# Kernel optimization log

Hardware: AMD Instinct MI355X
Metric: run time of the kernel (lower is better)

## Reference

```python
import jax, jax.numpy as jnp
import numpy as np

SHARPNESS_SIGMA = 0.75
EPS = 1e-17


def eps_denom(denom):
    # guard tiny denominators, preserving sign (sign of 0 treated as +1)
    sign = jnp.where(denom >= 0, 1.0, -1.0)
    return jnp.where(jnp.abs(denom) < EPS, sign * EPS, denom)


def setup_inputs() -> dict:
    key = jax.random.key(0)
    k1, k2 = jax.random.split(key)
    B, P, K = 4, 100000, 32
    normals = jax.random.normal(k1, (B, P, 3), dtype=jnp.float32)
    knn_idx = jax.random.randint(k2, (B, P, K), 0, P, dtype=jnp.int64)
    return {"normals": normals, "knn_idx": knn_idx}


def reference(normals, knn_idx):
    # knn_gather: [B,P,3] gathered at [B,P,K] -> [B,P,K,3]
    knn_normals = jax.vmap(lambda n, i: n[i])(normals, knn_idx)

    # get_normal_w: exp(-||n - ni||^2 / sigma^2) on unit normals
    inv_sigma = 1.0 / (SHARPNESS_SIGMA * SHARPNESS_SIGMA)
    n_unit = normals / eps_denom(jnp.linalg.norm(normals, axis=-1, keepdims=True))
    kn_unit = knn_normals / eps_denom(jnp.linalg.norm(knn_normals, axis=-1, keepdims=True))
    diff = kn_unit - n_unit[:, :, None, :]                      # [B,P,K,3]
    weights = jnp.exp(-jnp.sum(diff * diff, axis=-1) * inv_sigma)  # [B,P,K]

    # _denoise_normals: weighted average of (raw) neighbor normals
    num = jnp.sum(knn_normals * weights[:, :, :, None], axis=-2)   # [B,P,3]
    den = eps_denom(jnp.sum(weights, axis=-1, keepdims=True))      # [B,P,1]
    normals_denoised = num / den
    return normals_denoised
```

## Files before the change

### kernel.cpp

```cpp
#include <hip/hip_runtime.h>
#include <hip/hip_bf16.h>


#define SL_B 4
#define SL_P 100000
#define SL_K 32
#define SL_HALF 16
#define SL_INV_SIG2 1.77777779f
#define SL_EPS 1e-17f

__global__ __launch_bounds__(256) void SurfaceLoss_kernel(
    const float* __restrict__ normals,
    const int*   __restrict__ knn,
    float*       __restrict__ out)
{
    int gid = blockIdx.x * blockDim.x + threadIdx.x;
    int p = gid >> 1;
    if (p >= SL_B * SL_P) return;
    int h = gid & 1;
    int b = p / SL_P;
    int pl = p - b * SL_P;

    const float* nb = normals + (size_t)b * (SL_P * 3);

    {
    }
    int coff = pl * 3;
    bool clast = (pl == SL_P - 1);
    float4 cv = *reinterpret_cast<const float4*>(nb + (clast ? coff - 1 : coff));
    float nx = clast ? cv.y : cv.x;
    float ny = clast ? cv.z : cv.y;
    float nz = clast ? cv.w : cv.z;
    float ninv = 1.0f / fmaxf(sqrtf(nx * nx + ny * ny + nz * nz), SL_EPS);
    float ux = nx * ninv, uy = ny * ninv, uz = nz * ninv;

    int kid[SL_HALF];
    const int4* kp = reinterpret_cast<const int4*>(knn + (size_t)p * SL_K + h * SL_HALF);
#pragma unroll
    for (int j = 0; j < 4; ++j) {
        int4 q = kp[j];
        kid[4 * j + 0] = q.x;
        kid[4 * j + 1] = q.y;
        kid[4 * j + 2] = q.z;
        kid[4 * j + 3] = q.w;
    }

    float numx = 0.f, numy = 0.f, numz = 0.f, den = 0.f;

#pragma unroll
    for (int k = 0; k < SL_HALF; ++k) {
        int idx = kid[k];
        int off = idx * 3;
        bool last = (idx == SL_P - 1);
        float4 v = *reinterpret_cast<const float4*>(nb + (last ? off - 1 : off));
        float kx = last ? v.y : v.x;
        float ky = last ? v.z : v.y;
        float kz = last ? v.w : v.z;
        float kinv = 1.0f / fmaxf(sqrtf(kx * kx + ky * ky + kz * kz), SL_EPS);
        float dx = fmaf(kx, kinv, -ux);
        float dy = fmaf(ky, kinv, -uy);
        float dz = fmaf(kz, kinv, -uz);
        float d2 = dx * dx + dy * dy + dz * dz;
        float w = __expf(-d2 * SL_INV_SIG2);
        numx = fmaf(kx, w, numx);
        numy = fmaf(ky, w, numy);
        numz = fmaf(kz, w, numz);
        den += w;
    }

    numx += __shfl_xor(numx, 1);
    numy += __shfl_xor(numy, 1);
    numz += __shfl_xor(numz, 1);
    den  += __shfl_xor(den, 1);

    if (h == 0) {
        float dinv = 1.0f / fmaxf(den, SL_EPS);
        out[3 * (size_t)p + 0] = numx * dinv;
        out[3 * (size_t)p + 1] = numy * dinv;
        out[3 * (size_t)p + 2] = numz * dinv;
    }
}

extern "C" void kernel_launch(void* const* d_in, const int* in_sizes, int n_in,
                              void* d_out, int out_size, void* d_ws, size_t ws_size,
                              hipStream_t stream) {
    const float* normals = (const float*)d_in[0];
    const int*   knn     = (const int*)d_in[1];
    float*       out     = (float*)d_out;

    int total = SL_B * SL_P * 2;
    int block = 256;
    int grid = (total + block - 1) / block;
    SurfaceLoss_kernel<<<grid, block, 0, stream>>>(normals, knn, out);
}
```

Measured before the change: 71.49 us.

## Prepack normals into fp16 unit-vector plus length records for cheaper gathers

Adds a pre-pass that normalizes each normal once and stores the unit vector and length as four fp16 values in an 8-byte workspace record. The main kernel then gathers 8-byte records instead of 16-byte float4 loads, and computes the weight from a dot product (exp(2(d-1)/sigma^2)) with no per-neighbor sqrt or reciprocal. The goal is to cut gather bandwidth and per-neighbor ALU work, at the cost of an extra launch, reduced precision from fp16 storage, and weighted sums built from length times unit vector. A float32 fallback kernel runs when the workspace is too small.

```diff
diff --git a/kernel.cpp b/kernel.cpp
--- a/kernel.cpp
+++ b/kernel.cpp
@@ -1,38 +1,50 @@
 #include <hip/hip_runtime.h>
-#include <hip/hip_bf16.h>
+#include <hip/hip_fp16.h>
 
 
 #define SL_B 4
 #define SL_P 100000
 #define SL_K 32
 #define SL_HALF 16
-#define SL_INV_SIG2 1.77777779f
 #define SL_EPS 1e-17f
+#define SL_2INV 3.55555558f
 
-__global__ __launch_bounds__(256) void SurfaceLoss_kernel(
+union SlPk { float2 f; __half2 h[2]; };
+
+__global__ __launch_bounds__(256) void sl_pack(
     const float* __restrict__ normals,
-    const int*   __restrict__ knn,
-    float*       __restrict__ out)
+    float2* __restrict__ rec)
+{
+    int p = blockIdx.x * blockDim.x + threadIdx.x;
+    if (p >= SL_B * SL_P) return;
+    float nx = normals[3 * (size_t)p + 0];
+    float ny = normals[3 * (size_t)p + 1];
+    float nz = normals[3 * (size_t)p + 2];
+    float len = sqrtf(nx * nx + ny * ny + nz * nz);
+    float inv = 1.0f / fmaxf(len, SL_EPS);
+    SlPk pk;
+    pk.h[0] = __floats2half2_rn(nx * inv, ny * inv);
+    pk.h[1] = __floats2half2_rn(nz * inv, len);
+    rec[p] = pk.f;
+}
+
+__global__ __launch_bounds__(256) void sl_main(
+    const float2* __restrict__ rec,
+    const int*    __restrict__ knn,
+    float*        __restrict__ out)
 {
     int gid = blockIdx.x * blockDim.x + threadIdx.x;
     int p = gid >> 1;
     if (p >= SL_B * SL_P) return;
     int h = gid & 1;
     int b = p / SL_P;
+    const float2* rb = rec + (size_t)b * SL_P;
     int pl = p - b * SL_P;
 
-    const float* nb = normals + (size_t)b * (SL_P * 3);
-
-    {
-    }
-    int coff = pl * 3;
-    bool clast = (pl == SL_P - 1);
-    float4 cv = *reinterpret_cast<const float4*>(nb + (clast ? coff - 1 : coff));
-    float nx = clast ? cv.y : cv.x;
-    float ny = clast ? cv.z : cv.y;
-    float nz = clast ? cv.w : cv.z;
-    float ninv = 1.0f / fmaxf(sqrtf(nx * nx + ny * ny + nz * nz), SL_EPS);
-    float ux = nx * ninv, uy = ny * ninv, uz = nz * ninv;
+    SlPk cp; cp.f = rb[pl];
+    float ux = __low2float(cp.h[0]);
+    float uy = __high2float(cp.h[0]);
+    float uz = __low2float(cp.h[1]);
 
     int kid[SL_HALF];
     const int4* kp = reinterpret_cast<const int4*>(knn + (size_t)p * SL_K + h * SL_HALF);
@@ -49,22 +61,19 @@
 
 #pragma unroll
     for (int k = 0; k < SL_HALF; ++k) {
-        int idx = kid[k];
-        int off = idx * 3;
-        bool last = (idx == SL_P - 1);
-        float4 v = *reinterpret_cast<const float4*>(nb + (last ? off - 1 : off));
-        float kx = last ? v.y : v.x;
-        float ky = last ? v.z : v.y;
-        float kz = last ? v.w : v.z;
-        float kinv = 1.0f / fmaxf(sqrtf(kx * kx + ky * ky + kz * kz), SL_EPS);
-        float dx = fmaf(kx, kinv, -ux);
-        float dy = fmaf(ky, kinv, -uy);
-        float dz = fmaf(kz, kinv, -uz);
-        float d2 = dx * dx + dy * dy + dz * dz;
-        float w = __expf(-d2 * SL_INV_SIG2);
-        numx = fmaf(kx, w, numx);
-        numy = fmaf(ky, w, numy);
-        numz = fmaf(kz, w, numz);
+        SlPk pk; pk.f = rb[kid[k]];
+        float kx = __low2float(pk.h[0]);
+        float ky = __high2float(pk.h[0]);
+        float kz = __low2float(pk.h[1]);
+        float kl = __high2float(pk.h[1]);
+        float d = kx * ux;
+        d = fmaf(ky, uy, d);
+        d = fmaf(kz, uz, d);
+        float w = __expf(fmaf(d, SL_2INV, -SL_2INV));
+        float s = w * kl;
+        numx = fmaf(kx, s, numx);
+        numy = fmaf(ky, s, numy);
+        numz = fmaf(kz, s, numz);
         den += w;
     }
 
@@ -81,6 +90,69 @@
     }
 }
 
+__global__ __launch_bounds__(256) void sl_fallback(
+    const float* __restrict__ normals,
+    const int*   __restrict__ knn,
+    float*       __restrict__ out)
+{
+    int gid = blockIdx.x * blockDim.x + threadIdx.x;
+    int p = gid >> 1;
+    if (p >= SL_B * SL_P) return;
+    int h = gid & 1;
+    int b = p / SL_P;
+    int pl = p - b * SL_P;
+    const float* nb = normals + (size_t)b * (SL_P * 3);
+
+    int coff = pl * 3;
+    bool clast = (pl == SL_P - 1);
+    float4 cv = *reinterpret_cast<const float4*>(nb + (clast ? coff - 1 : coff));
+    float nx = clast ? cv.y : cv.x;
+    float ny = clast ? cv.z : cv.y;
+    float nz = clast ? cv.w : cv.z;
+    float ninv = 1.0f / fmaxf(sqrtf(nx * nx + ny * ny + nz * nz), SL_EPS);
+    float ux = nx * ninv, uy = ny * ninv, uz = nz * ninv;
+
+    int kid[SL_HALF];
+    const int4* kp = reinterpret_cast<const int4*>(knn + (size_t)p * SL_K + h * SL_HALF);
+#pragma unroll
+    for (int j = 0; j < 4; ++j) {
+        int4 q = kp[j];
+        kid[4 * j + 0] = q.x; kid[4 * j + 1] = q.y;
+        kid[4 * j + 2] = q.z; kid[4 * j + 3] = q.w;
+    }
+    float numx = 0.f, numy = 0.f, numz = 0.f, den = 0.f;
+#pragma unroll
+    for (int k = 0; k < SL_HALF; ++k) {
+        int idx = kid[k];
+        int off = idx * 3;
+        bool last = (idx == SL_P - 1);
+        float4 v = *reinterpret_cast<const float4*>(nb + (last ? off - 1 : off));
+        float kx = last ? v.y : v.x;
+        float ky = last ? v.z : v.y;
+        float kz = last ? v.w : v.z;
+        float kinv = 1.0f / fmaxf(sqrtf(kx * kx + ky * ky + kz * kz), SL_EPS);
+        float dx = fmaf(kx, kinv, -ux);
+        float dy = fmaf(ky, kinv, -uy);
+        float dz = fmaf(kz, kinv, -uz);
+        float d2 = dx * dx + dy * dy + dz * dz;
+        float w = __expf(-d2 * 1.77777779f);
+        numx = fmaf(kx, w, numx);
+        numy = fmaf(ky, w, numy);
+        numz = fmaf(kz, w, numz);
+        den += w;
+    }
+    numx += __shfl_xor(numx, 1);
+    numy += __shfl_xor(numy, 1);
+    numz += __shfl_xor(numz, 1);
+    den  += __shfl_xor(den, 1);
+    if (h == 0) {
+        float dinv = 1.0f / fmaxf(den, SL_EPS);
+        out[3 * (size_t)p + 0] = numx * dinv;
+        out[3 * (size_t)p + 1] = numy * dinv;
+        out[3 * (size_t)p + 2] = numz * dinv;
+    }
+}
+
 extern "C" void kernel_launch(void* const* d_in, const int* in_sizes, int n_in,
                               void* d_out, int out_size, void* d_ws, size_t ws_size,
                               hipStream_t stream) {
@@ -88,8 +160,15 @@
     const int*   knn     = (const int*)d_in[1];
     float*       out     = (float*)d_out;
 
-    int total = SL_B * SL_P * 2;
-    int block = 256;
-    int grid = (total + block - 1) / block;
-    SurfaceLoss_kernel<<<grid, block, 0, stream>>>(normals, knn, out);
+    const size_t need = (size_t)SL_B * SL_P * sizeof(float2);
+    if (ws_size >= need) {
+        float2* rec = (float2*)d_ws;
+        int n1 = SL_B * SL_P;
+        sl_pack<<<(n1 + 255) / 256, 256, 0, stream>>>(normals, rec);
+        int n2 = SL_B * SL_P * 2;
+        sl_main<<<(n2 + 255) / 256, 256, 0, stream>>>(rec, knn, out);
+    } else {
+        int n2 = SL_B * SL_P * 2;
+        sl_fallback<<<(n2 + 255) / 256, 256, 0, stream>>>(normals, knn, out);
+    }
 }
```

Result: faster. 66.79 us (-6.6%).
